# Optimization experiments

Measured on AMD Instinct MI355X. Metric: run time of the kernel, lower is better.

## Reference

```python
import jax, jax.numpy as jnp
import numpy as np

D_IN, D_OUT, D_K, D_V, H = 768, 768, 64, 64, 12


def setup_inputs() -> dict:
    key = jax.random.key(0)
    ks = jax.random.split(key, 16)
    b, nq, nk = 4, 1024, 1024
    inp = {
        'queries': jax.random.normal(ks[0], (b, nq, D_IN), jnp.float32),
        'keys': jax.random.normal(ks[1], (b, nk, D_IN), jnp.float32),
        'values': jax.random.normal(ks[2], (b, nk, D_IN), jnp.float32),
        'loss_map': jax.random.normal(ks[3], (b, nk, H), jnp.float32),
        'attention_mask': jax.random.randint(ks[4], (b, H, nq, nk), 0, 2).astype(bool),
        'attention_weights': jax.random.uniform(ks[5], (b, H, nq, nk), jnp.float32),
        # learned params (stored as (in, out); math-equivalent to torch Linear)
        'Wq': jax.random.normal(ks[6], (D_IN, H * D_K), jnp.float32) * 0.02,
        'bq': jnp.zeros((H * D_K,), jnp.float32),
        'Wk': jax.random.normal(ks[7], (D_IN, H * D_K), jnp.float32) * 0.02,
        'bk': jnp.zeros((H * D_K,), jnp.float32),
        'Wv': jax.random.normal(ks[8], (D_IN, H * D_V), jnp.float32) * 0.02,
        'bv': jnp.zeros((H * D_V,), jnp.float32),
        'Wo': jax.random.normal(ks[9], (H * D_V, D_OUT), jnp.float32) * 0.02,
        'bo': jnp.zeros((D_OUT,), jnp.float32),
    }
    return inp


def reference(queries, keys, values, loss_map, attention_mask, attention_weights,
              Wq, bq, Wk, bk, Wv, bv, Wo, bo):
    b, nq, _ = queries.shape
    nk = keys.shape[1]
    # projections -> (b, h, n, d)
    q = (queries @ Wq + bq).reshape(b, nq, H, D_K).transpose(0, 2, 1, 3)
    k = (keys @ Wk + bk).reshape(b, nk, H, D_K).transpose(0, 2, 1, 3)
    v = (values @ Wv + bv).reshape(b, nk, H, D_V).transpose(0, 2, 1, 3)
    # scaled scores (b, h, nq, nk)
    att = jnp.einsum('bhqd,bhkd->bhqk', q, k) / np.sqrt(D_K).astype(np.float32)
    att = att * attention_weights
    att = jnp.where(attention_mask, -jnp.inf, att)
    # additive per-key, per-head bias: loss_map (b, nk, h) -> (b, h, 1, nk)
    w_g = loss_map.transpose(0, 2, 1)[:, :, None, :]
    w_mn = jax.nn.softmax(att + w_g, axis=-1)
    # dropout is identity in eval / p=0
    out = jnp.einsum('bhqk,bhkd->bhqd', w_mn, v)
    out = out.transpose(0, 2, 1, 3).reshape(b, nq, H * D_V)
    return out @ Wo + bo
```

## Files before the change

### kernel.cpp

```cpp
#include <hip/hip_runtime.h>
#include <hip/hip_bf16.h>
#include <cmath>

static constexpr int HN = 12;
static constexpr int DHEAD = 64;
static constexpr int DMODEL = 768;
static constexpr int NQ = 1024;
static constexpr int NB = 4;
static constexpr int NCH = 4;
static constexpr int MROWS = NB * NQ;
static constexpr size_t PER = (size_t)NB * HN * NQ * DHEAD;
static constexpr size_t WN  = (size_t)DMODEL * DMODEL;
static constexpr size_t CHROWS = (size_t)NB * HN * NQ;

typedef __attribute__((ext_vector_type(8))) short bf16x8;
typedef __attribute__((ext_vector_type(4))) float f32x4;

static __device__ __forceinline__ unsigned short f2bf(float f) {
    unsigned int u = __builtin_bit_cast(unsigned int, f);
    unsigned int r = (u + 0x7FFFu + ((u >> 16) & 1u)) >> 16;
    return (unsigned short)r;
}
static __device__ __forceinline__ unsigned pack2(float lo, float hi) {
    return (unsigned)f2bf(lo) | ((unsigned)f2bf(hi) << 16);
}

typedef const __attribute__((address_space(1))) unsigned int gu32;
typedef __attribute__((address_space(3))) unsigned int lu32;
static __device__ __forceinline__ void gload16(const void* g, void* l) {
    __builtin_amdgcn_global_load_lds((gu32*)g, (lu32*)l, 16, 0, 0);
}

__global__ __launch_bounds__(256)
void cvt3(const float* __restrict__ a, const float* __restrict__ b, const float* __restrict__ c,
          unsigned short* __restrict__ oa, unsigned short* __restrict__ ob, unsigned short* __restrict__ oc)
{
    const int z = blockIdx.z;
    const float* s = z == 0 ? a : z == 1 ? b : c;
    unsigned short* d = z == 0 ? oa : z == 1 ? ob : oc;
    size_t i = ((size_t)blockIdx.x * 256 + threadIdx.x) * 4;
    float4 v = *(const float4*)&s[i];
    ushort4 u;
    u.x = f2bf(v.x); u.y = f2bf(v.y); u.z = f2bf(v.z); u.w = f2bf(v.w);
    *(ushort4*)&d[i] = u;
}

__global__ __launch_bounds__(256)
void wtrans(const float* __restrict__ w0, const float* __restrict__ w1,
            const float* __restrict__ w2, const float* __restrict__ w3,
            unsigned short* __restrict__ o0, unsigned short* __restrict__ o1,
            unsigned short* __restrict__ o2, unsigned short* __restrict__ o3)
{
    const int z = blockIdx.z;
    const float* in = z == 0 ? w0 : z == 1 ? w1 : z == 2 ? w2 : w3;
    unsigned short* out = z == 0 ? o0 : z == 1 ? o1 : z == 2 ? o2 : o3;
    __shared__ float t[64][65];
    const int tid = threadIdx.x;
    const int k0 = blockIdx.x * 64, n0 = blockIdx.y * 64;
    #pragma unroll
    for (int l = 0; l < 16; ++l) {
        int idx = l * 256 + tid, r = idx >> 6, cc = idx & 63;
        t[r][cc] = in[(size_t)(k0 + r) * DMODEL + n0 + cc];
    }
    __syncthreads();
    #pragma unroll
    for (int l = 0; l < 16; ++l) {
        int idx = l * 256 + tid, r = idx >> 6, cc = idx & 63;
        out[(size_t)(n0 + r) * DMODEL + k0 + cc] = f2bf(t[cc][r]);
    }
}

static __device__ __forceinline__
void gemm_body(const unsigned short* __restrict__ A, const unsigned short* __restrict__ Wt,
               const float* __restrict__ bias, void* __restrict__ C, int layout)
{
    constexpr int K = DMODEL;
    __shared__ unsigned short As[128 * 64];
    __shared__ unsigned short Bs[128 * 64];
    const int tid = threadIdx.x, w = tid >> 6, lane = tid & 63;
    const int c = lane & 15, g = lane >> 4;
    const int wr = w >> 1, wc = w & 1;
    const int bn = blockIdx.x * 128, bm = blockIdx.y * 128;

    f32x4 acc[4][4] = {};
    for (int k0 = 0; k0 < K; k0 += 64) {
        #pragma unroll
        for (int it = 0; it < 4; ++it) {
            int idx = it * 256 + tid, r = idx >> 3, blk = idx & 7;
            int so = (blk ^ (r & 7)) << 3;
            gload16(A  + (size_t)(bm + r) * K + k0 + so, &As[(it * 256 + w * 64) * 8]);
            gload16(Wt + (size_t)(bn + r) * K + k0 + so, &Bs[(it * 256 + w * 64) * 8]);
        }
        __syncthreads();
        #pragma unroll
        for (int kk = 0; kk < 2; ++kk) {
            bf16x8 a[4], b[4];
            #pragma unroll
            for (int mi = 0; mi < 4; ++mi) {
                int row = wr * 64 + mi * 16 + c;
                a[mi] = *(const bf16x8*)&As[row * 64 + ((((kk << 2) | g) ^ (row & 7)) << 3)];
            }
            #pragma unroll
            for (int ni = 0; ni < 4; ++ni) {
                int row = wc * 64 + ni * 16 + c;
                b[ni] = *(const bf16x8*)&Bs[row * 64 + ((((kk << 2) | g) ^ (row & 7)) << 3)];
            }
            #pragma unroll
            for (int mi = 0; mi < 4; ++mi)
                #pragma unroll
                for (int ni = 0; ni < 4; ++ni)
                    acc[mi][ni] = __builtin_amdgcn_mfma_f32_16x16x32_bf16(a[mi], b[ni], acc[mi][ni], 0, 0, 0);
        }
        __syncthreads();
    }

    #pragma unroll
    for (int ni = 0; ni < 4; ++ni) {
        int col = bn + wc * 64 + ni * 16 + c;
        float bvx = bias[col];
        int hh = col >> 6, d = col & 63;
        #pragma unroll
        for (int mi = 0; mi < 4; ++mi) {
            int m0 = bm + wr * 64 + mi * 16 + 4 * g;
            int bb = m0 >> 10, nn0 = m0 & (NQ - 1);
            if (layout == 0) {
                float* o = (float*)C;
                #pragma unroll
                for (int j = 0; j < 4; ++j)
                    o[(size_t)(m0 + j) * DMODEL + col] = acc[mi][ni][j] + bvx;
            } else if (layout == 1) {
                unsigned short* o = (unsigned short*)C;
                #pragma unroll
                for (int j = 0; j < 4; ++j)
                    o[(((size_t)bb * HN + hh) * NQ + nn0 + j) * DHEAD + d] =
                        f2bf(acc[mi][ni][j] + bvx);
            } else {
                unsigned short* o = (unsigned short*)C;
                ushort4 u;
                u.x = f2bf(acc[mi][ni][0] + bvx);
                u.y = f2bf(acc[mi][ni][1] + bvx);
                u.z = f2bf(acc[mi][ni][2] + bvx);
                u.w = f2bf(acc[mi][ni][3] + bvx);
                *(ushort4*)&o[(((size_t)bb * HN + hh) * DHEAD + d) * NQ + nn0] = u;
            }
        }
    }
}

__global__ __launch_bounds__(256)
void qkv_gemm(const unsigned short* __restrict__ qa, const unsigned short* __restrict__ ka,
              const unsigned short* __restrict__ va,
              const unsigned short* __restrict__ wq, const unsigned short* __restrict__ wk,
              const unsigned short* __restrict__ wv,
              const float* __restrict__ bq, const float* __restrict__ bk, const float* __restrict__ bv,
              unsigned short* __restrict__ qo, unsigned short* __restrict__ ko,
              unsigned short* __restrict__ vo)
{
    const int z = blockIdx.z;
    const unsigned short* A  = z == 0 ? qa : z == 1 ? ka : va;
    const unsigned short* Wt = z == 0 ? wq : z == 1 ? wk : wv;
    const float* bias        = z == 0 ? bq : z == 1 ? bk : bv;
    unsigned short* C        = z == 0 ? qo : z == 1 ? ko : vo;
    gemm_body(A, Wt, bias, C, z == 2 ? 2 : 1);
}

__global__ __launch_bounds__(256)
void o_gemm(const unsigned short* __restrict__ A, const unsigned short* __restrict__ Wt,
            const float* __restrict__ bias, float* __restrict__ C)
{
    gemm_body(A, Wt, bias, C, 0);
}

__global__ __launch_bounds__(256, 4)
void attn_part(const unsigned short* __restrict__ qws,
               const unsigned short* __restrict__ kws,
               const unsigned short* __restrict__ vtws,
               const float* __restrict__ aw, const int* __restrict__ mask,
               const float* __restrict__ lm,
               float* __restrict__ opart, float* __restrict__ mpart,
               float* __restrict__ lpart)
{
    const int qt = blockIdx.x, h = blockIdx.y;
    const int b = blockIdx.z >> 2, ch = blockIdx.z & 3;
    const int tid = threadIdx.x;
    const int w = tid >> 6, lane = tid & 63;
    const int c = lane & 15, g = lane >> 4;

    __shared__ unsigned short Ks[2][64 * 64];
    __shared__ unsigned short Vs[2][64 * 64];
    __shared__ float lms[256];

    const size_t bh = (size_t)b * HN + h;
    const unsigned short* qbase  = qws  + (bh * NQ + (size_t)qt * 64) * DHEAD;
    const unsigned short* kbase  = kws  + (bh * NQ + (size_t)ch * 256) * DHEAD;
    const unsigned short* vtbase = vtws + bh * DHEAD * NQ + ch * 256;

    lms[tid] = lm[((size_t)b * NQ + ch * 256 + tid) * HN + h];

    auto stageKV = [&](int kt, int bufi) {
        #pragma unroll
        for (int it = 0; it < 2; ++it) {
            int idx = it * 256 + tid, r = idx >> 3, blk = idx & 7;
            int so = (blk ^ (r & 7)) << 3;
            gload16(kbase + (size_t)(kt * 64 + r) * DHEAD + so, &Ks[bufi][(it * 256 + w * 64) * 8]);
            gload16(vtbase + (size_t)r * NQ + kt * 64 + so,     &Vs[bufi][(it * 256 + w * 64) * 8]);
        }
    };
    stageKV(0, 0);

    const int qrow = w * 16 + c;
    const bf16x8 qf0 = *(const bf16x8*)&qbase[qrow * DHEAD + g * 8];
    const bf16x8 qf1 = *(const bf16x8*)&qbase[qrow * DHEAD + 32 + g * 8];

    const size_t awbase = (bh * NQ + (size_t)(qt * 64 + qrow)) * NQ + ch * 256;

    f32x4 O[4] = {{0,0,0,0},{0,0,0,0},{0,0,0,0},{0,0,0,0}};
    float mrun = -1e30f, lrun = 0.f;
    const int srcl = c + ((g & 1) << 5);
    const bool hiT = (g >> 1) != 0;

    __syncthreads();

    #pragma unroll
    for (int kt = 0; kt < 4; ++kt) {
        const int cur = kt & 1;
        if (kt < 3) stageKV(kt + 1, cur ^ 1);

        float4 aw4[4]; int4 mk4[4]; float4 lm4[4];
        #pragma unroll
        for (int nt = 0; nt < 4; ++nt) {
            size_t o = awbase + kt * 64 + nt * 16 + 4 * g;
            aw4[nt] = *(const float4*)&aw[o];
            mk4[nt] = *(const int4*)&mask[o];
            lm4[nt] = *(const float4*)&lms[kt * 64 + nt * 16 + 4 * g];
        }

        f32x4 s[4] = {{0,0,0,0},{0,0,0,0},{0,0,0,0},{0,0,0,0}};
        #pragma unroll
        for (int kk = 0; kk < 2; ++kk) {
            bf16x8 qf = kk ? qf1 : qf0;
            #pragma unroll
            for (int nt = 0; nt < 4; ++nt) {
                bf16x8 kf = *(const bf16x8*)&Ks[cur][(nt * 16 + c) * 64 + ((((kk << 2) | g) ^ (c & 7)) << 3)];
                s[nt] = __builtin_amdgcn_mfma_f32_16x16x32_bf16(kf, qf, s[nt], 0, 0, 0);
            }
        }

        float p[4][4];
        float tmax = -INFINITY;
        #pragma unroll
        for (int nt = 0; nt < 4; ++nt) {
            const float* av = (const float*)&aw4[nt];
            const int*   mv = (const int*)&mk4[nt];
            const float* lv = (const float*)&lm4[nt];
            #pragma unroll
            for (int j = 0; j < 4; ++j) {
                float v = mv[j] ? -1e30f : fmaf(s[nt][j], 0.125f * av[j], lv[j]);
                p[nt][j] = v;
                tmax = fmaxf(tmax, v);
            }
        }
        tmax = fmaxf(tmax, __shfl_xor(tmax, 16));
        tmax = fmaxf(tmax, __shfl_xor(tmax, 32));

        float mn = fmaxf(mrun, tmax);
        float scal = __expf(mrun - mn);
        mrun = mn;
        float rs = 0.f;
        #pragma unroll
        for (int nt = 0; nt < 4; ++nt)
            #pragma unroll
            for (int j = 0; j < 4; ++j) {
                float e = __expf(p[nt][j] - mn);
                p[nt][j] = e;
                rs += e;
            }
        rs += __shfl_xor(rs, 16);
        rs += __shfl_xor(rs, 32);
        lrun = lrun * scal + rs;
        #pragma unroll
        for (int nd = 0; nd < 4; ++nd) O[nd] *= scal;

        int pk[4][2];
        #pragma unroll
        for (int nt = 0; nt < 4; ++nt) {
            pk[nt][0] = (int)pack2(p[nt][0], p[nt][1]);
            pk[nt][1] = (int)pack2(p[nt][2], p[nt][3]);
        }

        #pragma unroll
        for (int kk = 0; kk < 2; ++kk) {
            int xa0 = __shfl(pk[2 * kk][0], srcl),      xb0 = __shfl(pk[2 * kk + 1][0], srcl);
            int xa1 = __shfl(pk[2 * kk][1], srcl),      xb1 = __shfl(pk[2 * kk + 1][1], srcl);
            int xa2 = __shfl(pk[2 * kk][0], srcl + 16), xb2 = __shfl(pk[2 * kk + 1][0], srcl + 16);
            int xa3 = __shfl(pk[2 * kk][1], srcl + 16), xb3 = __shfl(pk[2 * kk + 1][1], srcl + 16);
            int4 bi;
            bi.x = hiT ? xb0 : xa0;
            bi.y = hiT ? xb1 : xa1;
            bi.z = hiT ? xb2 : xa2;
            bi.w = hiT ? xb3 : xa3;
            bf16x8 pa = __builtin_bit_cast(bf16x8, bi);
            #pragma unroll
            for (int nd = 0; nd < 4; ++nd) {
                bf16x8 vf = *(const bf16x8*)&Vs[cur][(nd * 16 + c) * 64 + ((((kk << 2) | g) ^ (c & 7)) << 3)];
                O[nd] = __builtin_amdgcn_mfma_f32_16x16x32_bf16(vf, pa, O[nd], 0, 0, 0);
            }
        }
        if (kt < 3) __syncthreads();
    }

    const size_t prow = ((size_t)(ch * NB + b) * HN + h) * NQ + qt * 64 + qrow;
    #pragma unroll
    for (int nd = 0; nd < 4; ++nd)
        *(f32x4*)&opart[prow * 64 + nd * 16 + 4 * g] = O[nd];
    if (g == 0) {
        mpart[prow] = mrun;
        lpart[prow] = lrun;
    }
}

__global__ __launch_bounds__(256)
void attn_combine(const float* __restrict__ opart, const float* __restrict__ mpart,
                  const float* __restrict__ lpart, unsigned short* __restrict__ out)
{
    const int qt = blockIdx.x, h = blockIdx.y, b = blockIdx.z;
    const int tid = threadIdx.x;
    const int q = qt * 64 + (tid >> 2);
    const int d0 = (tid & 3) * 16;
    const size_t row = ((size_t)b * HN + h) * NQ + q;

    float mv[4], lv[4];
    float M = -INFINITY;
    #pragma unroll
    for (int ci = 0; ci < 4; ++ci) {
        mv[ci] = mpart[ci * CHROWS + row];
        lv[ci] = lpart[ci * CHROWS + row];
        M = fmaxf(M, mv[ci]);
    }
    float L = 0.f;
    float wc[4];
    #pragma unroll
    for (int ci = 0; ci < 4; ++ci) {
        wc[ci] = __expf(mv[ci] - M);
        L += lv[ci] * wc[ci];
    }
    const float inv = 1.f / L;

    f32x4 o[4] = {{0,0,0,0},{0,0,0,0},{0,0,0,0},{0,0,0,0}};
    #pragma unroll
    for (int ci = 0; ci < 4; ++ci) {
        const float* src = opart + (ci * CHROWS + row) * 64 + d0;
        #pragma unroll
        for (int i = 0; i < 4; ++i) {
            f32x4 v = *(const f32x4*)&src[i * 4];
            o[i] += wc[ci] * v;
        }
    }
    const size_t ob = ((size_t)b * NQ + q) * DMODEL + h * DHEAD + d0;
    #pragma unroll
    for (int i = 0; i < 4; ++i) {
        ushort4 u;
        u.x = f2bf(o[i][0] * inv);
        u.y = f2bf(o[i][1] * inv);
        u.z = f2bf(o[i][2] * inv);
        u.w = f2bf(o[i][3] * inv);
        *(ushort4*)&out[ob + i * 4] = u;
    }
}

extern "C" void kernel_launch(void* const* d_in, const int* in_sizes, int n_in,
                              void* d_out, int out_size, void* d_ws, size_t ws_size,
                              hipStream_t stream)
{
    const float* queries = (const float*)d_in[0];
    const float* keys    = (const float*)d_in[1];
    const float* values  = (const float*)d_in[2];
    const float* lossmap = (const float*)d_in[3];
    const int*   mask    = (const int*)d_in[4];
    const float* aw      = (const float*)d_in[5];
    const float* Wq = (const float*)d_in[6];
    const float* bq = (const float*)d_in[7];
    const float* Wk = (const float*)d_in[8];
    const float* bk = (const float*)d_in[9];
    const float* Wv = (const float*)d_in[10];
    const float* bv = (const float*)d_in[11];
    const float* Wo = (const float*)d_in[12];
    const float* bo = (const float*)d_in[13];

    unsigned short* p = (unsigned short*)d_ws;
    unsigned short* qbf  = p; p += PER;
    unsigned short* kbf  = p; p += PER;
    unsigned short* vbf  = p; p += PER;
    unsigned short* qws  = p; p += PER;
    unsigned short* kws  = p; p += PER;
    unsigned short* vtws = p; p += PER;
    unsigned short* aobf = p; p += PER;
    unsigned short* wqt  = p; p += WN;
    unsigned short* wkt  = p; p += WN;
    unsigned short* wvt  = p; p += WN;
    unsigned short* wot  = p; p += WN;
    float* fp = (float*)p;
    float* opart = fp; fp += (size_t)NCH * CHROWS * 64;
    float* mpart = fp; fp += (size_t)NCH * CHROWS;
    float* lpart = fp; fp += (size_t)NCH * CHROWS;

    const int M = MROWS;
    cvt3<<<dim3((unsigned)(PER / 1024), 1, 3), 256, 0, stream>>>(queries, keys, values, qbf, kbf, vbf);
    wtrans<<<dim3(12, 12, 4), 256, 0, stream>>>(Wq, Wk, Wv, Wo, wqt, wkt, wvt, wot);
    qkv_gemm<<<dim3(DMODEL / 128, M / 128, 3), 256, 0, stream>>>(
        qbf, kbf, vbf, wqt, wkt, wvt, bq, bk, bv, qws, kws, vtws);
    attn_part<<<dim3(NQ / 64, HN, NB * NCH), 256, 0, stream>>>(
        qws, kws, vtws, aw, mask, lossmap, opart, mpart, lpart);
    attn_combine<<<dim3(NQ / 64, HN, NB), 256, 0, stream>>>(opart, mpart, lpart, aobf);
    o_gemm<<<dim3(DMODEL / 128, M / 128), 256, 0, stream>>>(aobf, wot, bo, (float*)d_out);
}
```

Baseline: 194.5 us.

## Double-buffer attention-weight and mask loads with explicit waitcnt and barriers

Attention-weight and mask tiles for the next key tile are now prefetched into alternating register sets, so the next tile's loads overlap the current tile's compute. The implicit __syncthreads is replaced by explicit s_waitcnt vmcnt(8) plus s_barrier with sched_barrier fences, which lets the in-flight prefetch loads stay outstanding across the barrier. MFMA sections are wrapped in s_setprio to raise wave priority. The manual vmcnt count must match the issued load order exactly, and the doubled register buffers raise register pressure.

```diff
diff --git a/kernel.cpp b/kernel.cpp
--- a/kernel.cpp
+++ b/kernel.cpp
@@ -195,8 +195,6 @@
     const unsigned short* kbase  = kws  + (bh * NQ + (size_t)ch * 256) * DHEAD;
     const unsigned short* vtbase = vtws + bh * DHEAD * NQ + ch * 256;
 
-    lms[tid] = lm[((size_t)b * NQ + ch * 256 + tid) * HN + h];
-
     auto stageKV = [&](int kt, int bufi) {
         #pragma unroll
         for (int it = 0; it < 2; ++it) {
@@ -206,36 +204,56 @@
             gload16(vtbase + (size_t)r * NQ + kt * 64 + so,     &Vs[bufi][(it * 256 + w * 64) * 8]);
         }
     };
-    stageKV(0, 0);
 
     const int qrow = w * 16 + c;
     const bf16x8 qf0 = *(const bf16x8*)&qbase[qrow * DHEAD + g * 8];
     const bf16x8 qf1 = *(const bf16x8*)&qbase[qrow * DHEAD + 32 + g * 8];
 
     const size_t awbase = (bh * NQ + (size_t)(qt * 64 + qrow)) * NQ + ch * 256;
+
+    auto prefetch = [&](int kt, float4 (&a4)[4], int4 (&m4)[4]) {
+        #pragma unroll
+        for (int nt = 0; nt < 4; ++nt) {
+            size_t o = awbase + kt * 64 + nt * 16 + 4 * g;
+            a4[nt] = *(const float4*)&aw[o];
+            m4[nt] = *(const int4*)&mask[o];
+        }
+    };
 
     f32x4 O[4] = {{0,0,0,0},{0,0,0,0},{0,0,0,0},{0,0,0,0}};
     float mrun = -1e30f, lrun = 0.f;
     const int srcl = c + ((g & 1) << 5);
     const bool hiT = (g >> 1) != 0;
 
-    __syncthreads();
-
-    #pragma unroll
-    for (int kt = 0; kt < 4; ++kt) {
+    float4 awA[4], awB[4];
+    int4   mkA[4], mkB[4];
+
+    lms[tid] = lm[((size_t)b * NQ + ch * 256 + tid) * HN + h];
+    stageKV(0, 0);
+    __builtin_amdgcn_sched_barrier(0);
+    prefetch(0, awA, mkA);
+    __builtin_amdgcn_sched_barrier(0);
+    asm volatile("s_waitcnt vmcnt(8) lgkmcnt(0)" ::: "memory");
+    __builtin_amdgcn_sched_barrier(0);
+    __builtin_amdgcn_s_barrier();
+    __builtin_amdgcn_sched_barrier(0);
+
+    auto body = [&](int kt, bool pref,
+                    float4 (&awC)[4], int4 (&mkC)[4],
+                    float4 (&awN)[4], int4 (&mkN)[4]) {
         const int cur = kt & 1;
-        if (kt < 3) stageKV(kt + 1, cur ^ 1);
-
-        float4 aw4[4]; int4 mk4[4]; float4 lm4[4];
-        #pragma unroll
-        for (int nt = 0; nt < 4; ++nt) {
-            size_t o = awbase + kt * 64 + nt * 16 + 4 * g;
-            aw4[nt] = *(const float4*)&aw[o];
-            mk4[nt] = *(const int4*)&mask[o];
+        if (pref) stageKV(kt + 1, cur ^ 1);
+        __builtin_amdgcn_sched_barrier(0);
+        if (pref) prefetch(kt + 1, awN, mkN);
+        __builtin_amdgcn_sched_barrier(0);
+
+        float4 lm4[4];
+        #pragma unroll
+        for (int nt = 0; nt < 4; ++nt)
             lm4[nt] = *(const float4*)&lms[kt * 64 + nt * 16 + 4 * g];
-        }
 
         f32x4 s[4] = {{0,0,0,0},{0,0,0,0},{0,0,0,0},{0,0,0,0}};
+        __builtin_amdgcn_s_setprio(1);
         #pragma unroll
         for (int kk = 0; kk < 2; ++kk) {
             bf16x8 qf = kk ? qf1 : qf0;
@@ -245,13 +263,14 @@
                 s[nt] = __builtin_amdgcn_mfma_f32_16x16x32_bf16(kf, qf, s[nt], 0, 0, 0);
             }
         }
+        __builtin_amdgcn_s_setprio(0);
 
         float p[4][4];
         float tmax = -INFINITY;
         #pragma unroll
         for (int nt = 0; nt < 4; ++nt) {
-            const float* av = (const float*)&aw4[nt];
-            const int*   mv = (const int*)&mk4[nt];
+            const float* av = (const float*)&awC[nt];
+            const int*   mv = (const int*)&mkC[nt];
             const float* lv = (const float*)&lm4[nt];
             #pragma unroll
             for (int j = 0; j < 4; ++j) {
@@ -300,14 +319,27 @@
             bi.z = hiT ? xb2 : xa2;
             bi.w = hiT ? xb3 : xa3;
             bf16x8 pa = __builtin_bit_cast(bf16x8, bi);
+            __builtin_amdgcn_s_setprio(1);
             #pragma unroll
             for (int nd = 0; nd < 4; ++nd) {
                 bf16x8 vf = *(const bf16x8*)&Vs[cur][(nd * 16 + c) * 64 + ((((kk << 2) | g) ^ (c & 7)) << 3)];
                 O[nd] = __builtin_amdgcn_mfma_f32_16x16x32_bf16(vf, pa, O[nd], 0, 0, 0);
             }
-        }
-        if (kt < 3) __syncthreads();
-    }
+            __builtin_amdgcn_s_setprio(0);
+        }
+
+        if (pref) {
+            asm volatile("s_waitcnt vmcnt(8) lgkmcnt(0)" ::: "memory");
+            __builtin_amdgcn_sched_barrier(0);
+            __builtin_amdgcn_s_barrier();
+            __builtin_amdgcn_sched_barrier(0);
+        }
+    };
+
+    body(0, true,  awA, mkA, awB, mkB);
+    body(1, true,  awB, mkB, awA, mkA);
+    body(2, true,  awA, mkA, awB, mkB);
+    body(3, false, awB, mkB, awA, mkA);
 
     const size_t prow = ((size_t)(ch * NB + b) * HN + h) * NQ + qt * 64 + qrow;
     #pragma unroll
```

After: 227.2 us. 16.8% more time.
